# Optimization experiments

Hardware: AMD Instinct MI355X
Metric: run time of the kernel (lower is better)

The kernel has to match this reference:

```python
import jax, jax.numpy as jnp
import numpy as np

D_MODEL = 512
N_HEADS = 8
D_K = D_MODEL // N_HEADS
D_DTW = 21


def setup_inputs() -> dict:
    key = jax.random.key(0)
    ks = jax.random.split(key, 16)
    bs, S = 16, 512
    def lin(k, fan_in, shape):
        return jax.random.uniform(k, shape, jnp.float32, -1.0, 1.0) / np.sqrt(fan_in)
    return {
        "Q": jax.random.normal(ks[0], (bs, S, D_MODEL), jnp.float32),
        "K": jax.random.normal(ks[1], (bs, S, D_MODEL), jnp.float32),
        "V": jax.random.normal(ks[2], (bs, S, D_MODEL), jnp.float32),
        "G": jax.random.normal(ks[3], (bs, S, D_MODEL), jnp.float32),
        "dtw_cost": jax.random.uniform(ks[4], (bs, D_DTW, S, S), jnp.float32),
        "Wq": lin(ks[5], D_MODEL, (D_MODEL, D_MODEL)), "bq": lin(ks[6], D_MODEL, (D_MODEL,)),
        "Wk": lin(ks[7], D_MODEL, (D_MODEL, D_MODEL)), "bk": lin(ks[8], D_MODEL, (D_MODEL,)),
        "Wv": lin(ks[9], D_MODEL, (D_MODEL, D_MODEL)), "bv": lin(ks[10], D_MODEL, (D_MODEL,)),
        "Wd": lin(ks[11], D_DTW, (N_HEADS, D_DTW)), "bd": lin(ks[12], D_DTW, (N_HEADS,)),
        "Wo": lin(ks[13], D_MODEL, (D_MODEL, D_MODEL)), "bo": lin(ks[14], D_MODEL, (D_MODEL,)),
    }


def reference(Q, K, V, G, dtw_cost, Wq, bq, Wk, bk, Wv, bv, Wd, bd, Wo, bo):
    bs, S, _ = Q.shape
    # QKV projections, split into heads: [bs, H, S, dk]
    def proj(x, W, b):
        y = x @ W.T + b
        return y.reshape(bs, S, N_HEADS, D_K).transpose(0, 2, 1, 3)
    q = proj(Q, Wq, bq)
    k = proj(K, Wk, bk)
    v = proj(V, Wv, bv)
    # scaled dot-product scores [bs, H, S, S]
    scores = jnp.einsum("bhqd,bhkd->bhqk", q, k) / np.sqrt(D_K).astype(np.float32)
    # DTW-cost bias: linear over the cost-channel dim (21 -> H), added per head
    bias = jnp.einsum("bcqk,hc->bhqk", dtw_cost, Wd) + bd[None, :, None, None]
    attn = jax.nn.softmax(scores + bias, axis=-1)
    out = jnp.einsum("bhqk,bhkd->bhqd", attn, v)  # [bs, H, S, dk]
    concat = out.transpose(0, 2, 1, 3).reshape(bs, S, D_MODEL)
    output = concat @ Wo.T + bo
    return (output, attn)
```

## Files before the change

### kernel.cpp

```cpp
#include <hip/hip_runtime.h>
#include <hip/hip_bf16.h>
#include <cstddef>
#include <cstdint>

#define BS   16
#define SLEN 512
#define DM   512
#define NH   8
#define DK   64
#define DC   21

typedef __attribute__((ext_vector_type(8))) short short8;
typedef __attribute__((ext_vector_type(4))) float f32x4;
typedef __attribute__((ext_vector_type(4))) _Float16 h16x4;

__device__ inline unsigned pack_bf16(float a, float b) {
    unsigned ua = __builtin_bit_cast(unsigned, a);
    unsigned ub = __builtin_bit_cast(unsigned, b);
    ua = (ua + 0x7fffu + ((ua >> 16) & 1u)) >> 16;
    ub = (ub + 0x7fffu + ((ub >> 16) & 1u)) >> 16;
    return ua | (ub << 16);
}
__device__ inline unsigned cvt2(float a, float b) { return pack_bf16(a, b); }
__device__ inline ushort bf16_1(float a) { return (ushort)(pack_bf16(a, 0.f) & 0xffffu); }

__device__ __host__ inline size_t bias_chunk_base(int bh, int q16) {
    return 2 * (((size_t)bh * SLEN + (size_t)q16) * SLEN);
}

template<int MODE>
__global__ __launch_bounds__(256) void gemm_bf16(
    const void* __restrict__ Xv, const float* __restrict__ W,
    const float* __restrict__ bias, void* __restrict__ outv)
{
    __shared__ alignas(16) ushort Atile[64 * 64];
    __shared__ alignas(16) ushort Btile[128 * 64];

    const float*  Xf = (const float*)Xv;
    const ushort* Xb = (const ushort*)Xv;

    const int tid = threadIdx.x;
    const int wave = tid >> 6, lane = tid & 63;
    const int lq = lane & 15, lg = lane >> 4;
    const int wr = wave >> 1, wc = wave & 1;
    const int m0 = blockIdx.x * 64;
    const int n0 = blockIdx.y * 128;

    f32x4 acc[2][4];
#pragma unroll
    for (int i = 0; i < 2; ++i)
#pragma unroll
        for (int j = 0; j < 4; ++j) acc[i][j] = (f32x4){0.f, 0.f, 0.f, 0.f};

    float4 pa[2][2], pb[4][2];
    uint4  qa[2];

#define LOAD_A(K0)                                                              \
    if (MODE == 3) {                                                            \
        _Pragma("unroll")                                                       \
        for (int i = 0; i < 2; ++i) {                                           \
            const int P = tid + 256 * i;                                        \
            const int row = P >> 3, sl = P & 7;                                 \
            qa[i] = *(const uint4*)&Xb[(size_t)(m0 + row) * 512 + (K0) + sl * 8]; \
        }                                                                       \
    } else {                                                                    \
        _Pragma("unroll")                                                       \
        for (int i = 0; i < 2; ++i) {                                           \
            const int P = tid + 256 * i;                                        \
            const int row = P >> 3, cp = P & 7;                                 \
            const float4* s = (const float4*)&Xf[(size_t)(m0 + row) * 512 + (K0) + cp * 8]; \
            pa[i][0] = s[0]; pa[i][1] = s[1];                                   \
        }                                                                       \
    }
#define LOAD_B(K0)                                                              \
    _Pragma("unroll")                                                           \
    for (int i = 0; i < 4; ++i) {                                               \
        const int P = tid + 256 * i;                                            \
        const int row = P >> 3, cp = P & 7;                                     \
        const float4* s = (const float4*)&W[(size_t)(n0 + row) * 512 + (K0) + cp * 8]; \
        pb[i][0] = s[0]; pb[i][1] = s[1];                                       \
    }

    LOAD_A(0)
    LOAD_B(0)

    for (int it = 0; it < 8; ++it) {
        __syncthreads();
        if (MODE == 3) {
#pragma unroll
            for (int i = 0; i < 2; ++i) {
                const int P = tid + 256 * i;
                const int row = P >> 3, sl = P & 7;
                *(uint4*)((char*)Atile + row * 128 + 16 * (sl ^ (row & 7))) = qa[i];
            }
        } else {
#pragma unroll
            for (int i = 0; i < 2; ++i) {
                const int P = tid + 256 * i;
                const int row = P >> 3, cp = P & 7;
                uint4 w;
                w.x = cvt2(pa[i][0].x, pa[i][0].y);
                w.y = cvt2(pa[i][0].z, pa[i][0].w);
                w.z = cvt2(pa[i][1].x, pa[i][1].y);
                w.w = cvt2(pa[i][1].z, pa[i][1].w);
                *(uint4*)((char*)Atile + row * 128 + 16 * (cp ^ (row & 7))) = w;
            }
        }
#pragma unroll
        for (int i = 0; i < 4; ++i) {
            const int P = tid + 256 * i;
            const int row = P >> 3, cp = P & 7;
            uint4 w;
            w.x = cvt2(pb[i][0].x, pb[i][0].y);
            w.y = cvt2(pb[i][0].z, pb[i][0].w);
            w.z = cvt2(pb[i][1].x, pb[i][1].y);
            w.w = cvt2(pb[i][1].z, pb[i][1].w);
            *(uint4*)((char*)Btile + row * 128 + 16 * (cp ^ (row & 7))) = w;
        }
        __syncthreads();

        if (it < 7) {
            const int kn = (it + 1) * 64;
            LOAD_A(kn)
            LOAD_B(kn)
        }

        short8 af[2][2], bfr[4][2];
#pragma unroll
        for (int mi = 0; mi < 2; ++mi)
#pragma unroll
            for (int kh = 0; kh < 2; ++kh) {
                const int row = wr * 32 + mi * 16 + lq;
                af[mi][kh] = *(const short8*)((const char*)Atile + row * 128 +
                                              16 * ((kh * 4 + lg) ^ (row & 7)));
            }
#pragma unroll
        for (int ni = 0; ni < 4; ++ni)
#pragma unroll
            for (int kh = 0; kh < 2; ++kh) {
                const int row = wc * 64 + ni * 16 + lq;
                bfr[ni][kh] = *(const short8*)((const char*)Btile + row * 128 +
                                               16 * ((kh * 4 + lg) ^ (row & 7)));
            }
        __builtin_amdgcn_s_setprio(1);
#pragma unroll
        for (int kh = 0; kh < 2; ++kh)
#pragma unroll
            for (int mi = 0; mi < 2; ++mi)
#pragma unroll
                for (int ni = 0; ni < 4; ++ni)
                    acc[mi][ni] = __builtin_amdgcn_mfma_f32_16x16x32_bf16(
                        af[mi][kh], bfr[ni][kh], acc[mi][ni], 0, 0, 0);
        __builtin_amdgcn_s_setprio(0);
    }
#undef LOAD_A
#undef LOAD_B

    if (MODE == 3) {
        float* out = (float*)outv;
#pragma unroll
        for (int mi = 0; mi < 2; ++mi) {
            const int mb = m0 + wr * 32 + mi * 16 + lg * 4;
#pragma unroll
            for (int ni = 0; ni < 4; ++ni) {
                const int n = n0 + wc * 64 + ni * 16 + lq;
                const float bb = bias[n];
#pragma unroll
                for (int r = 0; r < 4; ++r)
                    out[(size_t)(mb + r) * 512 + n] = acc[mi][ni][r] + bb;
            }
        }
    } else if (MODE == 1) {
        ushort* out = (ushort*)outv;
#pragma unroll
        for (int mi = 0; mi < 2; ++mi) {
            const int mb = m0 + wr * 32 + mi * 16 + lg * 4;
#pragma unroll
            for (int ni = 0; ni < 4; ++ni) {
                const int n = n0 + wc * 64 + ni * 16 + lq;
                const int h = n >> 6, d = n & 63;
                const float bb = bias[n];
#pragma unroll
                for (int r = 0; r < 4; ++r) {
                    const int m = mb + r;
                    const int bidx = m >> 9, s = m & 511;
                    out[((size_t)(bidx * NH + h) * SLEN + s) * DK + d] =
                        bf16_1(acc[mi][ni][r] + bb);
                }
            }
        }
    } else {
        ushort* out = (ushort*)outv;
#pragma unroll
        for (int mi = 0; mi < 2; ++mi) {
            const int mb = m0 + wr * 32 + mi * 16 + lg * 4;
            const int bidx = mb >> 9, s0 = mb & 511;
#pragma unroll
            for (int ni = 0; ni < 4; ++ni) {
                const int n = n0 + wc * 64 + ni * 16 + lq;
                const int h = n >> 6, d = n & 63;
                const float bb = bias[n];
                uint2 pk;
                pk.x = cvt2(acc[mi][ni][0] + bb, acc[mi][ni][1] + bb);
                pk.y = cvt2(acc[mi][ni][2] + bb, acc[mi][ni][3] + bb);
                *(uint2*)&out[((size_t)(bidx * NH + h) * DK + d) * SLEN + s0] = pk;
            }
        }
    }
}

__global__ __launch_bounds__(512) void bias_kernel(
    const float* __restrict__ dtw, const float* __restrict__ Wd,
    const float* __restrict__ bd, _Float16* __restrict__ bias16)
{
    __shared__ float wdl[NH * DC];
    __shared__ float bdl[NH];
    const int k = threadIdx.x;
    const int q = blockIdx.x;
    const int b = blockIdx.y;
    if (k < NH * DC) wdl[k] = Wd[k];
    if (k < NH) bdl[k] = bd[k];
    __syncthreads();

    float acc[NH];
#pragma unroll
    for (int h = 0; h < NH; ++h) acc[h] = bdl[h];

    const float* p = dtw + ((size_t)b * DC * SLEN + q) * SLEN + k;
#pragma unroll
    for (int c = 0; c < DC; ++c) {
        const float x = p[(size_t)c * SLEN * SLEN];
#pragma unroll
        for (int h = 0; h < NH; ++h) acc[h] += x * wdl[h * DC + c];
    }
    const int q16 = q & ~15, ql = q & 15;
#pragma unroll
    for (int h = 0; h < NH; ++h) {
        const size_t base = bias_chunk_base(b * NH + h, q16);
        bias16[base + (size_t)ql * SLEN + k] = (_Float16)acc[h];
    }
}

__global__ __launch_bounds__(256, 2) void attn_mfma(
    const ushort* __restrict__ qb, const ushort* __restrict__ kb,
    const ushort* __restrict__ vt, float* __restrict__ attn,
    ushort* __restrict__ concat)
{
    __shared__ ushort P_lds[4][16][512];

    const int tid = threadIdx.x;
    const int wave = tid >> 6;
    const int lane = tid & 63;
    const int lq = lane & 15;
    const int lg = lane >> 4;

    const unsigned l = blockIdx.x;
    const int g  = (int)((l & 7) + 8 * (l >> 6));
    const int qt = (int)((l >> 3) & 7);
    const int h = g & 7, b = g >> 3;
    const int bh = b * NH + h;
    const int q0 = qt * 64 + wave * 16;

    const ushort* qptr = qb + ((size_t)bh * SLEN + q0) * DK;
    const ushort* kptr = kb + (size_t)bh * SLEN * DK;
    const ushort* vptr = vt + (size_t)bh * DK * SLEN;
    float* attn_b = attn + ((size_t)bh * SLEN + q0) * SLEN;
    const _Float16* bias_row =
        (const _Float16*)attn + bias_chunk_base(bh, q0) + (size_t)lq * SLEN;

    const short8 qf0 = *(const short8*)&qptr[(size_t)lq * DK + lg * 8];
    const short8 qf1 = *(const short8*)&qptr[(size_t)lq * DK + lg * 8 + 32];

    f32x4 sc[32];
#pragma unroll
    for (int kt = 0; kt < 32; ++kt) {
        const short8 a0 = *(const short8*)&kptr[(size_t)(kt * 16 + lq) * DK + lg * 8];
        const short8 a1 = *(const short8*)&kptr[(size_t)(kt * 16 + lq) * DK + lg * 8 + 32];
        f32x4 c = {0.f, 0.f, 0.f, 0.f};
        __builtin_amdgcn_s_setprio(1);
        c = __builtin_amdgcn_mfma_f32_16x16x32_bf16(a0, qf0, c, 0, 0, 0);
        c = __builtin_amdgcn_mfma_f32_16x16x32_bf16(a1, qf1, c, 0, 0, 0);
        __builtin_amdgcn_s_setprio(0);
        const h16x4 bh4 = *(const h16x4*)&bias_row[kt * 16 + lg * 4];
        f32x4 bias4;
        bias4[0] = (float)bh4[0]; bias4[1] = (float)bh4[1];
        bias4[2] = (float)bh4[2]; bias4[3] = (float)bh4[3];
        sc[kt] = c * 0.125f + bias4;
    }

    float m = -1e30f;
#pragma unroll
    for (int kt = 0; kt < 32; ++kt)
        m = fmaxf(m, fmaxf(fmaxf(sc[kt][0], sc[kt][1]), fmaxf(sc[kt][2], sc[kt][3])));
    m = fmaxf(m, __shfl_xor(m, 16));
    m = fmaxf(m, __shfl_xor(m, 32));

    float sum = 0.f;
#pragma unroll
    for (int kt = 0; kt < 32; ++kt) {
        f32x4 e;
        e[0] = __expf(sc[kt][0] - m);
        e[1] = __expf(sc[kt][1] - m);
        e[2] = __expf(sc[kt][2] - m);
        e[3] = __expf(sc[kt][3] - m);
        sum += (e[0] + e[1]) + (e[2] + e[3]);
        sc[kt] = e;
    }
    sum += __shfl_xor(sum, 16);
    sum += __shfl_xor(sum, 32);
    const float inv = 1.0f / sum;

    char* pbase = (char*)&P_lds[wave][0][0];
    const unsigned swz = (unsigned)((lq & 7) << 4);
#pragma unroll
    for (int kt = 0; kt < 32; ++kt) {
        const f32x4 e = sc[kt];
        f32x4 a4 = e * inv;
        *(f32x4*)&attn_b[(size_t)lq * SLEN + kt * 16 + lg * 4] = a4;
        uint2 pk;
        pk.x = pack_bf16(e[0], e[1]);
        pk.y = pack_bf16(e[2], e[3]);
        const unsigned byte = (unsigned)(lq * 1024 + kt * 32 + lg * 8) ^ swz;
        *(uint2*)(pbase + byte) = pk;
    }
    asm volatile("s_waitcnt lgkmcnt(0)" ::: "memory");
    __builtin_amdgcn_sched_barrier(0);

    f32x4 oacc[4] = {{0.f,0.f,0.f,0.f},{0.f,0.f,0.f,0.f},{0.f,0.f,0.f,0.f},{0.f,0.f,0.f,0.f}};
#pragma unroll
    for (int c = 0; c < 16; ++c) {
        const unsigned byteA = (unsigned)(lq * 1024 + c * 64 + lg * 16) ^ swz;
        const short8 pa = *(const short8*)(pbase + byteA);
        __builtin_amdgcn_s_setprio(1);
#pragma unroll
        for (int dt = 0; dt < 4; ++dt) {
            const short8 vb8 = *(const short8*)&vptr[(size_t)(dt * 16 + lq) * SLEN + c * 32 + lg * 8];
            oacc[dt] = __builtin_amdgcn_mfma_f32_16x16x32_bf16(pa, vb8, oacc[dt], 0, 0, 0);
        }
        __builtin_amdgcn_s_setprio(0);
    }

    ushort* cbase = concat + ((size_t)(b * SLEN + q0)) * DM + h * 64;
#pragma unroll
    for (int r = 0; r < 4; ++r) {
        const float iv = __shfl(inv, lg * 4 + r);
#pragma unroll
        for (int dt = 0; dt < 4; ++dt) {
            cbase[(size_t)(lg * 4 + r) * DM + dt * 16 + lq] = bf16_1(oacc[dt][r] * iv);
        }
    }
}

extern "C" void kernel_launch(void* const* d_in, const int* in_sizes, int n_in,
                              void* d_out, int out_size, void* d_ws, size_t ws_size,
                              hipStream_t stream)
{
    const float* Q   = (const float*)d_in[0];
    const float* K   = (const float*)d_in[1];
    const float* V   = (const float*)d_in[2];
    const float* dtw = (const float*)d_in[4];
    const float* Wq  = (const float*)d_in[5];
    const float* bq  = (const float*)d_in[6];
    const float* Wk  = (const float*)d_in[7];
    const float* bk  = (const float*)d_in[8];
    const float* Wv  = (const float*)d_in[9];
    const float* bv  = (const float*)d_in[10];
    const float* Wd  = (const float*)d_in[11];
    const float* bd  = (const float*)d_in[12];
    const float* Wo  = (const float*)d_in[13];
    const float* bo  = (const float*)d_in[14];

    float* out  = (float*)d_out;
    float* attn = out + (size_t)BS * SLEN * DM;
    _Float16* bias16 = (_Float16*)attn;

    const size_t PHS = (size_t)BS * NH * SLEN * DK;
    ushort* qb = (ushort*)d_ws;
    ushort* kb = qb + PHS;
    ushort* vt = kb + PHS;
    ushort* cb = vt + PHS;

    const dim3 gemm_grid(128, 4);

    gemm_bf16<1><<<gemm_grid, 256, 0, stream>>>(Q, Wq, bq, qb);
    gemm_bf16<1><<<gemm_grid, 256, 0, stream>>>(K, Wk, bk, kb);
    gemm_bf16<2><<<gemm_grid, 256, 0, stream>>>(V, Wv, bv, vt);

    bias_kernel<<<dim3(SLEN, BS), 512, 0, stream>>>(dtw, Wd, bd, bias16);

    attn_mfma<<<dim3(1024), 256, 0, stream>>>(qb, kb, vt, attn, cb);

    gemm_bf16<3><<<gemm_grid, 256, 0, stream>>>(cb, Wo, bo, out);
}
```

Baseline: 269.9 us.

## Recompute scores in two passes to drop register-held scores and raise occupancy

The attention kernel no longer keeps all 32 score tiles in registers. A first pass computes the exp-sum, and a second pass recomputes QK^T plus bias, writes normalized attn and feeds P through a small double-buffered LDS tile into the PV MFMA. It also skips max subtraction, switches P and V to fp16 (V written as f16 by the GEMM), reorganizes the bias layout into 32-wide segments, and raises launch bounds to 3 blocks per CU. This trades a doubled QK MFMA and bias read for lower register and LDS pressure, and risks overflow because the max is no longer subtracted.

Result: slower. 299.6 us (+11.0%).

```diff
diff --git a/kernel.cpp b/kernel.cpp
--- a/kernel.cpp
+++ b/kernel.cpp
@@ -12,7 +12,8 @@
 
 typedef __attribute__((ext_vector_type(8))) short short8;
 typedef __attribute__((ext_vector_type(4))) float f32x4;
-typedef __attribute__((ext_vector_type(4))) _Float16 h16x4;
+typedef __attribute__((ext_vector_type(8))) _Float16 h16x8;
+typedef _Float16 h16x4a __attribute__((ext_vector_type(4), may_alias));
 
 __device__ inline unsigned pack_bf16(float a, float b) {
     unsigned ua = __builtin_bit_cast(unsigned, a);
@@ -23,6 +24,9 @@
 }
 __device__ inline unsigned cvt2(float a, float b) { return pack_bf16(a, b); }
 __device__ inline ushort bf16_1(float a) { return (ushort)(pack_bf16(a, 0.f) & 0xffffu); }
+__device__ inline unsigned pk_f16(float a, float b) {
+    return __builtin_bit_cast(unsigned, __builtin_amdgcn_cvt_pkrtz(a, b));
+}
 
 __device__ __host__ inline size_t bias_chunk_base(int bh, int q16) {
     return 2 * (((size_t)bh * SLEN + (size_t)q16) * SLEN);
@@ -201,8 +205,8 @@
                 const int h = n >> 6, d = n & 63;
                 const float bb = bias[n];
                 uint2 pk;
-                pk.x = cvt2(acc[mi][ni][0] + bb, acc[mi][ni][1] + bb);
-                pk.y = cvt2(acc[mi][ni][2] + bb, acc[mi][ni][3] + bb);
+                pk.x = pk_f16(acc[mi][ni][0] + bb, acc[mi][ni][1] + bb);
+                pk.y = pk_f16(acc[mi][ni][2] + bb, acc[mi][ni][3] + bb);
                 *(uint2*)&out[((size_t)(bidx * NH + h) * DK + d) * SLEN + s0] = pk;
             }
         }
@@ -234,19 +238,20 @@
         for (int h = 0; h < NH; ++h) acc[h] += x * wdl[h * DC + c];
     }
     const int q16 = q & ~15, ql = q & 15;
+    const size_t seg = 1024 * (size_t)ql + 64 * (size_t)(k >> 5) + (k & 31);
 #pragma unroll
     for (int h = 0; h < NH; ++h) {
         const size_t base = bias_chunk_base(b * NH + h, q16);
-        bias16[base + (size_t)ql * SLEN + k] = (_Float16)acc[h];
-    }
-}
-
-__global__ __launch_bounds__(256, 2) void attn_mfma(
+        bias16[base + seg] = (_Float16)acc[h];
+    }
+}
+
+__global__ __launch_bounds__(256, 3) void attn_mfma(
     const ushort* __restrict__ qb, const ushort* __restrict__ kb,
     const ushort* __restrict__ vt, float* __restrict__ attn,
     ushort* __restrict__ concat)
 {
-    __shared__ ushort P_lds[4][16][512];
+    __shared__ alignas(16) ushort Pbuf[4][2][16][32];
 
     const int tid = threadIdx.x;
     const int wave = tid >> 6;
@@ -266,76 +271,70 @@
     const ushort* vptr = vt + (size_t)bh * DK * SLEN;
     float* attn_b = attn + ((size_t)bh * SLEN + q0) * SLEN;
     const _Float16* bias_row =
-        (const _Float16*)attn + bias_chunk_base(bh, q0) + (size_t)lq * SLEN;
+        (const _Float16*)attn + bias_chunk_base(bh, q0) + 1024 * (size_t)lq;
 
     const short8 qf0 = *(const short8*)&qptr[(size_t)lq * DK + lg * 8];
     const short8 qf1 = *(const short8*)&qptr[(size_t)lq * DK + lg * 8 + 32];
 
-    f32x4 sc[32];
-#pragma unroll
+    float sum = 0.f;
+#pragma unroll 8
     for (int kt = 0; kt < 32; ++kt) {
         const short8 a0 = *(const short8*)&kptr[(size_t)(kt * 16 + lq) * DK + lg * 8];
         const short8 a1 = *(const short8*)&kptr[(size_t)(kt * 16 + lq) * DK + lg * 8 + 32];
         f32x4 c = {0.f, 0.f, 0.f, 0.f};
-        __builtin_amdgcn_s_setprio(1);
         c = __builtin_amdgcn_mfma_f32_16x16x32_bf16(a0, qf0, c, 0, 0, 0);
         c = __builtin_amdgcn_mfma_f32_16x16x32_bf16(a1, qf1, c, 0, 0, 0);
-        __builtin_amdgcn_s_setprio(0);
-        const h16x4 bh4 = *(const h16x4*)&bias_row[kt * 16 + lg * 4];
-        f32x4 bias4;
-        bias4[0] = (float)bh4[0]; bias4[1] = (float)bh4[1];
-        bias4[2] = (float)bh4[2]; bias4[3] = (float)bh4[3];
-        sc[kt] = c * 0.125f + bias4;
-    }
-
-    float m = -1e30f;
-#pragma unroll
-    for (int kt = 0; kt < 32; ++kt)
-        m = fmaxf(m, fmaxf(fmaxf(sc[kt][0], sc[kt][1]), fmaxf(sc[kt][2], sc[kt][3])));
-    m = fmaxf(m, __shfl_xor(m, 16));
-    m = fmaxf(m, __shfl_xor(m, 32));
-
-    float sum = 0.f;
-#pragma unroll
-    for (int kt = 0; kt < 32; ++kt) {
-        f32x4 e;
-        e[0] = __expf(sc[kt][0] - m);
-        e[1] = __expf(sc[kt][1] - m);
-        e[2] = __expf(sc[kt][2] - m);
-        e[3] = __expf(sc[kt][3] - m);
-        sum += (e[0] + e[1]) + (e[2] + e[3]);
-        sc[kt] = e;
+        const h16x4a b4 = *(const h16x4a*)&bias_row[64 * (kt >> 1) + 16 * (kt & 1) + 4 * lg];
+        const float s0 = c[0] * 0.125f + (float)b4[0];
+        const float s1 = c[1] * 0.125f + (float)b4[1];
+        const float s2 = c[2] * 0.125f + (float)b4[2];
+        const float s3 = c[3] * 0.125f + (float)b4[3];
+        sum += (__expf(s0) + __expf(s1)) + (__expf(s2) + __expf(s3));
     }
     sum += __shfl_xor(sum, 16);
     sum += __shfl_xor(sum, 32);
     const float inv = 1.0f / sum;
 
-    char* pbase = (char*)&P_lds[wave][0][0];
-    const unsigned swz = (unsigned)((lq & 7) << 4);
-#pragma unroll
-    for (int kt = 0; kt < 32; ++kt) {
-        const f32x4 e = sc[kt];
-        f32x4 a4 = e * inv;
-        *(f32x4*)&attn_b[(size_t)lq * SLEN + kt * 16 + lg * 4] = a4;
-        uint2 pk;
-        pk.x = pack_bf16(e[0], e[1]);
-        pk.y = pack_bf16(e[2], e[3]);
-        const unsigned byte = (unsigned)(lq * 1024 + kt * 32 + lg * 8) ^ swz;
-        *(uint2*)(pbase + byte) = pk;
-    }
-    asm volatile("s_waitcnt lgkmcnt(0)" ::: "memory");
-    __builtin_amdgcn_sched_barrier(0);
-
     f32x4 oacc[4] = {{0.f,0.f,0.f,0.f},{0.f,0.f,0.f,0.f},{0.f,0.f,0.f,0.f},{0.f,0.f,0.f,0.f}};
-#pragma unroll
-    for (int c = 0; c < 16; ++c) {
-        const unsigned byteA = (unsigned)(lq * 1024 + c * 64 + lg * 16) ^ swz;
-        const short8 pa = *(const short8*)(pbase + byteA);
+
+#pragma unroll 2
+    for (int c2 = 15; c2 >= 0; --c2) {
+        f32x4 ev[2];
+#pragma unroll
+        for (int t = 0; t < 2; ++t) {
+            const int kt = 2 * c2 + t;
+            const short8 a0 = *(const short8*)&kptr[(size_t)(kt * 16 + lq) * DK + lg * 8];
+            const short8 a1 = *(const short8*)&kptr[(size_t)(kt * 16 + lq) * DK + lg * 8 + 32];
+            f32x4 c = {0.f, 0.f, 0.f, 0.f};
+            c = __builtin_amdgcn_mfma_f32_16x16x32_bf16(a0, qf0, c, 0, 0, 0);
+            c = __builtin_amdgcn_mfma_f32_16x16x32_bf16(a1, qf1, c, 0, 0, 0);
+            const h16x4a b4 = *(const h16x4a*)&bias_row[64 * c2 + 16 * t + 4 * lg];
+            ev[t][0] = __expf(c[0] * 0.125f + (float)b4[0]);
+            ev[t][1] = __expf(c[1] * 0.125f + (float)b4[1]);
+            ev[t][2] = __expf(c[2] * 0.125f + (float)b4[2]);
+            ev[t][3] = __expf(c[3] * 0.125f + (float)b4[3]);
+        }
+#pragma unroll
+        for (int t = 0; t < 2; ++t)
+            *(f32x4*)&attn_b[(size_t)lq * SLEN + (2 * c2 + t) * 16 + lg * 4] = ev[t] * inv;
+
+        char* pb = (char*)&Pbuf[wave][c2 & 1][0][0];
+#pragma unroll
+        for (int t = 0; t < 2; ++t) {
+            uint2 pk;
+            pk.x = pk_f16(ev[t][0], ev[t][1]);
+            pk.y = pk_f16(ev[t][2], ev[t][3]);
+            const int slot = (t * 2 + (lg >> 1)) ^ (lq & 3);
+            *(uint2*)(pb + lq * 64 + slot * 16 + (lg & 1) * 8) = pk;
+        }
+        asm volatile("s_waitcnt lgkmcnt(0)" ::: "memory");
+
+        const h16x8 pa = *(const h16x8*)(pb + lq * 64 + (lg ^ (lq & 3)) * 16);
         __builtin_amdgcn_s_setprio(1);
 #pragma unroll
         for (int dt = 0; dt < 4; ++dt) {
-            const short8 vb8 = *(const short8*)&vptr[(size_t)(dt * 16 + lq) * SLEN + c * 32 + lg * 8];
-            oacc[dt] = __builtin_amdgcn_mfma_f32_16x16x32_bf16(pa, vb8, oacc[dt], 0, 0, 0);
+            const h16x8 vb8 = *(const h16x8*)&vptr[(size_t)(dt * 16 + lq) * SLEN + c2 * 32 + lg * 8];
+            oacc[dt] = __builtin_amdgcn_mfma_f32_16x16x32_f16(pa, vb8, oacc[dt], 0, 0, 0);
         }
         __builtin_amdgcn_s_setprio(0);
     }
```
